# Performance work log

Hardware: AMD Instinct MI355X
Metric: run time of the kernel (lower is better)

Reference implementation:

```python
import jax, jax.numpy as jnp
import numpy as np

N = 40000          # nodes
E = 400000         # edges (avg degree 10)
MUL0, MUL1 = 64, 32   # 64x0e + 32x1o
RAD, HID = 8, 64      # fc_neurons = [8, 64]
WNUM = 192            # tp.weight_numel = 64+64+32+32
NUM_NEIGHBORS = 10.0
INV3 = 1.0 / np.sqrt(3.0)   # wigner coeff for 1o x 1o -> 0e


def _lin(s, v, Ws, Wv, attr):
    """FullyConnectedTensorProduct(x, 1x0e attr) == per-irrep linear, fan-in normalized."""
    out_s = (s @ Ws) * attr * (1.0 / np.sqrt(Ws.shape[0]))
    out_v = jnp.einsum('nud,uv->nvd', v, Wv) * attr[..., None] * (1.0 / np.sqrt(Wv.shape[0]))
    return out_s, out_v


def setup_inputs() -> dict:
    key = jax.random.key(0)
    ks = jax.random.split(key, 16)
    return {
        'node_input':   jax.random.normal(ks[0], (N, MUL0 + 3 * MUL1), jnp.float32),
        'node_attr':    jnp.ones((N, 1), jnp.float32),
        'edge_attr':    jax.random.normal(ks[1], (E, 4), jnp.float32),   # 1x0e + 1x1o
        'edge_scalars': jax.random.uniform(ks[2], (E, RAD), jnp.float32),
        'W_sc_s': jax.random.normal(ks[3], (MUL0, MUL0), jnp.float32),
        'W_sc_v': jax.random.normal(ks[4], (MUL1, MUL1), jnp.float32),
        'W1_s':   jax.random.normal(ks[5], (MUL0, MUL0), jnp.float32),
        'W1_v':   jax.random.normal(ks[6], (MUL1, MUL1), jnp.float32),
        'W2_s':   jax.random.normal(ks[7], (MUL0 + MUL1, MUL0), jnp.float32),
        'W2_v':   jax.random.normal(ks[8], (MUL0 + MUL1, MUL1), jnp.float32),
        'W3':     jax.random.normal(ks[9], (MUL0 + MUL1, 1), jnp.float32),
        'fcW1':   jax.random.normal(ks[10], (RAD, HID), jnp.float32),
        'fcW2':   jax.random.normal(ks[11], (HID, WNUM), jnp.float32),
        'edge_src': jax.random.randint(ks[12], (E,), 0, N, jnp.int32),
        'edge_dst': jax.random.randint(ks[13], (E,), 0, N, jnp.int32),
    }


def reference(node_input, node_attr, edge_attr, edge_scalars,
              W_sc_s, W_sc_v, W1_s, W1_v, W2_s, W2_v, W3, fcW1, fcW2,
              edge_src, edge_dst):
    n = node_input.shape[0]
    s_in = node_input[:, :MUL0]                       # (N, 64)   0e
    v_in = node_input[:, MUL0:].reshape(n, MUL1, 3)   # (N, 32,3) 1o

    # self connection + first linear (FCTP with 1x0e attr)
    sc_s, sc_v = _lin(s_in, v_in, W_sc_s, W_sc_v, node_attr)
    f_s,  f_v  = _lin(s_in, v_in, W1_s,  W1_v,  node_attr)

    # radial MLP -> per-edge tensor-product weights (silu, fan-in normalized)
    h = jax.nn.silu(edge_scalars @ fcW1 * (1.0 / np.sqrt(RAD)))
    w = h @ fcW2 * (1.0 / np.sqrt(HID))               # (E, 192)
    wA, wB, wC, wD = w[:, :64], w[:, 64:128], w[:, 128:160], w[:, 160:192]

    # gather source node features
    xs = f_s[edge_src]                                # (E, 64)
    xv = f_v[edge_src]                                # (E, 32, 3)
    y0 = edge_attr[:, :1]                             # (E, 1)  0e
    y1 = edge_attr[:, 1:4]                            # (E, 3)  1o

    # 'uvu' tensor-product paths -> irreps_mid = 64x0e + 32x0e + 64x1o + 32x1o
    outA = wA * xs * y0                                            # 0e x 0e -> 0e
    outD = wD * jnp.einsum('eud,ed->eu', xv, y1) * INV3            # 1o x 1o -> 0e
    outB = wB[:, :, None] * xs[:, :, None] * y1[:, None, :]       # 0e x 1o -> 1o
    outC = wC[:, :, None] * xv * y0[:, :, None]                    # 1o x 0e -> 1o
    edge_feat = jnp.concatenate(
        [outA, outD, outB.reshape(-1, MUL0 * 3), outC.reshape(-1, MUL1 * 3)], axis=1)  # (E, 384)

    # scatter_add into destination nodes, normalized by sqrt(num_neighbors)
    agg = jax.ops.segment_sum(edge_feat, edge_dst, num_segments=n)
    agg = agg * (1.0 / np.sqrt(NUM_NEIGHBORS))

    ms = agg[:, :MUL0 + MUL1]                               # (N, 96)   0e
    mv = agg[:, MUL0 + MUL1:].reshape(n, MUL0 + MUL1, 3)    # (N, 96,3) 1o

    # lin2: mid -> output ; lin3: mid -> 0e (scalars only)
    c_s, c_v = _lin(ms, mv, W2_s, W2_v, node_attr)
    conv = jnp.concatenate([c_s, c_v.reshape(n, -1)], axis=1)
    sc   = jnp.concatenate([sc_s, sc_v.reshape(n, -1)], axis=1)
    angle = 0.1 * (ms @ W3) * node_attr * (1.0 / np.sqrt(MUL0 + MUL1))  # (N, 1)

    # sc.output_mask is all-ones here (every output irrep has a path)
    cos, sin = jnp.cos(angle), jnp.sin(angle)
    return cos * sc + sin * conv
```

## Files before the change

kernel.cpp:

```cpp
#include <hip/hip_runtime.h>
#include <math.h>

#define MUL0 64
#define MUL1 32
#define RADF 8
#define HIDF 64
#define WNUM 192
#define NODE_F 160
#define AGG_F  384
#define SWS 200

#define INV_SQRT64 0.125f
#define INV_SQRT32 0.17677669529663687f
#define INV_SQRT8  0.35355339059327373f
#define INV_SQRT96 0.10206207261596575f
#define INV_SQRT10 0.31622776601683794f
#define INV_SQRT3  0.5773502691896258f

typedef __attribute__((ext_vector_type(8))) short bf16x8;
typedef __attribute__((ext_vector_type(4))) float f32x4;

__device__ __forceinline__ float bf2f(unsigned short u) {
    return __uint_as_float((unsigned)u << 16);
}
__device__ __forceinline__ unsigned short f2bfu(float x) {
    unsigned ua = __float_as_uint(x);
    return (unsigned short)((ua + 0x7FFF + ((ua >> 16) & 1)) >> 16);
}
__device__ __forceinline__ unsigned bf16pack(float a, float b) {
    unsigned ua = __float_as_uint(a);
    unsigned ub = __float_as_uint(b);
    ua = (ua + 0x7FFF + ((ua >> 16) & 1)) >> 16;
    ub = (ub + 0x7FFF + ((ub >> 16) & 1)) >> 16;
    return ua | (ub << 16);
}
__device__ __forceinline__ int rdlane(int v, int i) {
    return __builtin_amdgcn_readlane(v, i);
}
__device__ __forceinline__ bf16x8 cvt8(float4 a, float4 b) {
    union { unsigned q[4]; bf16x8 v; } r;
    r.q[0] = bf16pack(a.x, a.y);
    r.q[1] = bf16pack(a.z, a.w);
    r.q[2] = bf16pack(b.x, b.y);
    r.q[3] = bf16pack(b.z, b.w);
    return r.v;
}
__device__ __forceinline__ bf16x8 load8ovfb(const unsigned short* agn,
                                            const unsigned short* ovf16,
                                            int tA, int tB, int base)
{
    bf16x8 v = *(const bf16x8*)(agn + base);
    if (tA <= tB) {
        const unsigned short* pv = (const unsigned short*)&v;
        float f[8];
        #pragma unroll
        for (int j = 0; j < 8; ++j) f[j] = bf2f(pv[j]);
        for (int t = tA; t <= tB; ++t) {
            const unsigned short* ov = ovf16 + (size_t)t * AGG_F + base;
            #pragma unroll
            for (int j = 0; j < 8; ++j) f[j] += bf2f(ov[j]);
        }
        v = cvt8(make_float4(f[0], f[1], f[2], f[3]),
                 make_float4(f[4], f[5], f[6], f[7]));
    }
    return v;
}

__global__ __launch_bounds__(256) void k_node_lin(
    const float* __restrict__ node_input,
    const float* __restrict__ node_attr,
    const float* __restrict__ W1_s,
    const float* __restrict__ W1_v,
    unsigned short* __restrict__ f, int N)
{
    __shared__ unsigned short s_w1s[8 * 64 * 8];
    __shared__ unsigned short s_w1v[4 * 32 * 8];
    int tid = threadIdx.x;

    for (int task = tid; task < 8 * 64; task += 256) {
        int col = task & 63, koct = task >> 6;
        const float* wp = W1_s + (size_t)(koct * 8) * MUL0 + col;
        unsigned pk0 = bf16pack(wp[0 * MUL0] * INV_SQRT64, wp[1 * MUL0] * INV_SQRT64);
        unsigned pk1 = bf16pack(wp[2 * MUL0] * INV_SQRT64, wp[3 * MUL0] * INV_SQRT64);
        unsigned pk2 = bf16pack(wp[4 * MUL0] * INV_SQRT64, wp[5 * MUL0] * INV_SQRT64);
        unsigned pk3 = bf16pack(wp[6 * MUL0] * INV_SQRT64, wp[7 * MUL0] * INV_SQRT64);
        *(uint4*)&s_w1s[task * 8] = make_uint4(pk0, pk1, pk2, pk3);
    }
    for (int task = tid; task < 4 * 32; task += 256) {
        int col = task & 31, koct = task >> 5;
        const float* wp = W1_v + (size_t)(koct * 8) * MUL1 + col;
        unsigned pk0 = bf16pack(wp[0 * MUL1] * INV_SQRT32, wp[1 * MUL1] * INV_SQRT32);
        unsigned pk1 = bf16pack(wp[2 * MUL1] * INV_SQRT32, wp[3 * MUL1] * INV_SQRT32);
        unsigned pk2 = bf16pack(wp[4 * MUL1] * INV_SQRT32, wp[5 * MUL1] * INV_SQRT32);
        unsigned pk3 = bf16pack(wp[6 * MUL1] * INV_SQRT32, wp[7 * MUL1] * INV_SQRT32);
        *(uint4*)&s_w1v[task * 8] = make_uint4(pk0, pk1, pk2, pk3);
    }
    __syncthreads();

    int lane = tid & 63;
    int wv = tid >> 6;
    int l15 = lane & 15, lh = lane >> 4;
    int ntiles = (N + 15) >> 4;

    for (int tile = blockIdx.x * 4 + wv; tile < ntiles; tile += gridDim.x * 4) {
        int n0 = tile << 4;
        int m = min(16, N - n0);
        int nrow = n0 + min(l15, m - 1);
        const float* inn = node_input + (size_t)nrow * NODE_F;

        float attr[4];
        #pragma unroll
        for (int r = 0; r < 4; ++r)
            attr[r] = node_attr[n0 + min(lh * 4 + r, m - 1)];

        bf16x8 inS[2];
        #pragma unroll
        for (int kk = 0; kk < 2; ++kk) {
            const float* p0 = inn + kk * 32 + lh * 8;
            inS[kk] = cvt8(*(const float4*)p0, *(const float4*)(p0 + 4));
        }
        #pragma unroll
        for (int cb = 0; cb < 4; ++cb) {
            f32x4 a = {0.f, 0.f, 0.f, 0.f};
            #pragma unroll
            for (int kk = 0; kk < 2; ++kk) {
                bf16x8 b = *(const bf16x8*)&s_w1s[(((kk * 4 + lh) * 64) + cb * 16 + l15) * 8];
                a = __builtin_amdgcn_mfma_f32_16x16x32_bf16(inS[kk], b, a, 0, 0, 0);
            }
            #pragma unroll
            for (int r = 0; r < 4; ++r) {
                int node = lh * 4 + r;
                if (node < m)
                    f[(size_t)(n0 + node) * NODE_F + cb * 16 + l15] = f2bfu(a[r] * attr[r]);
            }
        }

        #pragma unroll
        for (int d = 0; d < 3; ++d) {
            float t[8];
            #pragma unroll
            for (int j = 0; j < 8; ++j)
                t[j] = inn[64 + (lh * 8 + j) * 3 + d];
            bf16x8 inV = cvt8(make_float4(t[0], t[1], t[2], t[3]),
                              make_float4(t[4], t[5], t[6], t[7]));
            #pragma unroll
            for (int cb = 0; cb < 2; ++cb) {
                bf16x8 b = *(const bf16x8*)&s_w1v[((lh * 32) + cb * 16 + l15) * 8];
                f32x4 a = {0.f, 0.f, 0.f, 0.f};
                a = __builtin_amdgcn_mfma_f32_16x16x32_bf16(inV, b, a, 0, 0, 0);
                #pragma unroll
                for (int r = 0; r < 4; ++r) {
                    int node = lh * 4 + r;
                    if (node < m)
                        f[(size_t)(n0 + node) * NODE_F + 64 + d * 32 + cb * 16 + l15] =
                            f2bfu(a[r] * attr[r]);
                }
            }
        }
    }
}

__global__ void k_count(const int* __restrict__ edge_dst, int* deg, int E)
{
    int e = blockIdx.x * blockDim.x + threadIdx.x;
    if (e < E) atomicAdd(&deg[edge_dst[e]], 1);
}

__global__ __launch_bounds__(1024) void k_scan_a(const int* __restrict__ deg,
                                                 int* __restrict__ off,
                                                 int* __restrict__ bsum, int N)
{
    __shared__ int swsum[16];
    __shared__ int swoff[16];
    __shared__ int stot;
    int lane = threadIdx.x & 63, wid = threadIdx.x >> 6;
    int ng4 = (N + 3) >> 2;
    int g = blockIdx.x * 1024 + threadIdx.x;
    int4 v = make_int4(0, 0, 0, 0);
    if (g < ng4) v = ((const int4*)deg)[g];
    int s = v.x + v.y + v.z + v.w;
    int val = s;
    #pragma unroll
    for (int sh = 1; sh < 64; sh <<= 1) {
        int t = __shfl_up(val, sh);
        if (lane >= sh) val += t;
    }
    if (lane == 63) swsum[wid] = val;
    __syncthreads();
    if (threadIdx.x < 16) {
        int x = swsum[threadIdx.x];
        int xv = x;
        #pragma unroll
        for (int sh = 1; sh < 16; sh <<= 1) {
            int t = __shfl_up(xv, sh);
            if ((int)threadIdx.x >= sh) xv += t;
        }
        swoff[threadIdx.x] = xv - x;
        if (threadIdx.x == 15) stot = xv;
    }
    __syncthreads();
    if (g < ng4) {
        int b0 = swoff[wid] + (val - s);
        int4 o;
        o.x = b0; o.y = b0 + v.x; o.z = o.y + v.y; o.w = o.z + v.z;
        ((int4*)off)[g] = o;
    }
    if (threadIdx.x == 0) bsum[blockIdx.x] = stot;
}

__global__ __launch_bounds__(1024) void k_scan_b(int* __restrict__ off,
                                                 int* __restrict__ cur,
                                                 const int* __restrict__ bsum,
                                                 unsigned short* __restrict__ agg,
                                                 const int* __restrict__ deg,
                                                 int N, int nb)
{
    __shared__ int sbase;
    if (threadIdx.x == 0) {
        int s = 0;
        for (int j = 0; j < (int)blockIdx.x; ++j) s += bsum[j];
        sbase = s;
    }
    __syncthreads();
    int base = sbase;
    int ng4 = (N + 3) >> 2;
    int g = blockIdx.x * 1024 + threadIdx.x;
    if (g < ng4) {
        int4 o = ((int4*)off)[g];
        o.x += base; o.y += base; o.z += base; o.w += base;
        ((int4*)off)[g] = o;
        ((int4*)cur)[g] = o;
        int4 d = ((const int4*)deg)[g];
        int n0 = g * 4;
        #pragma unroll
        for (int q = 0; q < 4; ++q) {
            int dq = (q == 0) ? d.x : (q == 1) ? d.y : (q == 2) ? d.z : d.w;
            int nq = n0 + q;
            if (dq == 0 && nq < N) {
                uint4* row = (uint4*)(agg + (size_t)nq * AGG_F);
                uint4 z = make_uint4(0, 0, 0, 0);
                for (int j = 0; j < AGG_F * 2 / 16; ++j) row[j] = z;
            }
        }
    }
}

__global__ void k_scatter(const int* __restrict__ edge_dst,
                          int* cur, int* __restrict__ csr, int E)
{
    int e = blockIdx.x * blockDim.x + threadIdx.x;
    if (e < E) {
        int d = edge_dst[e];
        int pos = atomicAdd(&cur[d], 1);
        csr[pos] = e;
    }
}

#define FLUSH_AGG(node, OVF)                                         \
    do {                                                             \
        unsigned short* an = (OVF) ? (ovf16 + (size_t)wt * AGG_F)    \
                                   : (agg + (size_t)(node) * AGG_F); \
        an[lane] = f2bfu(accA);                                      \
        an[96  + lane] = f2bfu(accB0);                               \
        an[192 + lane] = f2bfu(accB1);                               \
        an[288 + lane] = f2bfu(accB2);                               \
        if (lane < 32) {                                             \
            an[160 + u] = f2bfu(accX0);                              \
            an[256 + u] = f2bfu(accX1);                              \
            an[352 + u] = f2bfu(accX2);                              \
        } else {                                                     \
            an[64 + u] = f2bfu(accX0);                               \
        }                                                            \
    } while (0)

__global__ __launch_bounds__(512, 2) void k_edge_fused(
    const unsigned short* __restrict__ f,
    const float* __restrict__ edge_scalars,
    const float* __restrict__ edge_attr,
    const float* __restrict__ fcW1,
    const float* __restrict__ fcW2,
    const int* __restrict__ edge_src,
    const int* __restrict__ edge_dst,
    const int* __restrict__ csr,
    const int* __restrict__ off,
    unsigned short* __restrict__ agg,
    unsigned short* __restrict__ ovf16, int E)
{
    __shared__ unsigned short s_w2t[8 * 192 * 8];
    __shared__ unsigned short s_w[8][16 * SWS];
    __shared__ float s_fcW1[512];
    __shared__ float4 s_ea8[8][16];

    int tid  = threadIdx.x;
    int lane = tid & 63;
    int wv   = tid >> 6;
    int l15  = lane & 15, lh = lane >> 4;
    int u    = lane & 31;

    for (int task = tid; task < 1536; task += 512) {
        int col = task % 192, oct = task / 192;
        const float* wp = fcW2 + (size_t)(oct * 8) * WNUM + col;
        unsigned pk0 = bf16pack(wp[0 * WNUM], wp[1 * WNUM]);
        unsigned pk1 = bf16pack(wp[2 * WNUM], wp[3 * WNUM]);
        unsigned pk2 = bf16pack(wp[4 * WNUM], wp[5 * WNUM]);
        unsigned pk3 = bf16pack(wp[6 * WNUM], wp[7 * WNUM]);
        *(uint4*)&s_w2t[oct * 1536 + col * 8] = make_uint4(pk0, pk1, pk2, pk3);
    }
    for (int i = tid; i < 512; i += 512)
        s_fcW1[i] = fcW1[i];
    __syncthreads();

    unsigned short* sw = s_w[wv];
    float4* sea = s_ea8[wv];
    int nwt = (E + 15) >> 4;
    int stride8 = gridDim.x * 8;

    int wt = blockIdx.x * 8 + wv;
    if (wt >= nwt) return;

    int P = wt << 4;
    int m = min(16, E - P);
    int e0 = csr[P + min(l15, m - 1)];
    int src = edge_src[e0];
    int dst = edge_dst[e0];
    float4 ea = *(const float4*)(edge_attr + (size_t)e0 * 4);
    float4 es0, es1;
    {
        const float4* esp = (const float4*)(edge_scalars + (size_t)e0 * RADF);
        es0 = esp[0]; es1 = esp[1];
    }

    while (true) {
        if (lh == 0) sea[l15] = ea;

        int firstd = rdlane(dst, 0);
        int off_first = off[firstd];

        int wt_n = wt + stride8;
        bool hn = wt_n < nwt;
        int P_n = hn ? (wt_n << 4) : 0;
        int m_n = hn ? min(16, E - P_n) : 1;

        int e_n = csr[hn ? (P_n + min(l15, m_n - 1)) : 0];

        float xs[16], xv0[16], xv1[16], xv2[16];
        #pragma unroll
        for (int i = 0; i < 16; ++i) {
            int si = rdlane(src, i);
            const unsigned short* fb = f + (size_t)si * NODE_F;
            xs[i]  = bf2f(fb[lane]);
            xv0[i] = bf2f(fb[64 + u]);
            xv1[i] = bf2f(fb[96 + u]);
            xv2[i] = bf2f(fb[128 + u]);
        }

        float es[8] = {es0.x, es0.y, es0.z, es0.w, es1.x, es1.y, es1.z, es1.w};
        union { unsigned q[4]; bf16x8 v; } A0, A1;
        #pragma unroll
        for (int jp = 0; jp < 4; ++jp) {
            int k0 = lh * 8 + 2 * jp;
            float aL0 = 0.f, aL1 = 0.f, aH0 = 0.f, aH1 = 0.f;
            #pragma unroll
            for (int r = 0; r < 8; ++r) {
                float2 wl = *(const float2*)&s_fcW1[r * 64 + k0];
                float2 wh = *(const float2*)&s_fcW1[r * 64 + 32 + k0];
                aL0 = fmaf(es[r], wl.x, aL0);
                aL1 = fmaf(es[r], wl.y, aL1);
                aH0 = fmaf(es[r], wh.x, aH0);
                aH1 = fmaf(es[r], wh.y, aH1);
            }
            aL0 *= INV_SQRT8; aL1 *= INV_SQRT8; aH0 *= INV_SQRT8; aH1 *= INV_SQRT8;
            aL0 = aL0 / (1.f + __expf(-aL0));
            aL1 = aL1 / (1.f + __expf(-aL1));
            aH0 = aH0 / (1.f + __expf(-aH0));
            aH1 = aH1 / (1.f + __expf(-aH1));
            A0.q[jp] = bf16pack(aL0, aL1);
            A1.q[jp] = bf16pack(aH0, aH1);
        }

        int src_n = edge_src[e_n];
        int dst_n = edge_dst[e_n];
        float4 ea_n = *(const float4*)(edge_attr + (size_t)e_n * 4);
        float4 es0_n, es1_n;
        {
            const float4* espn = (const float4*)(edge_scalars + (size_t)e_n * RADF);
            es0_n = espn[0]; es1_n = espn[1];
        }

        #pragma unroll
        for (int cb = 0; cb < 12; ++cb) {
            bf16x8 b0 = *(const bf16x8*)&s_w2t[ lh      * 1536 + (cb * 16 + l15) * 8];
            bf16x8 b1 = *(const bf16x8*)&s_w2t[(4 + lh) * 1536 + (cb * 16 + l15) * 8];
            f32x4 acc = {0.f, 0.f, 0.f, 0.f};
            acc = __builtin_amdgcn_mfma_f32_16x16x32_bf16(A0.v, b0, acc, 0, 0, 0);
            acc = __builtin_amdgcn_mfma_f32_16x16x32_bf16(A1.v, b1, acc, 0, 0, 0);
            #pragma unroll
            for (int r = 0; r < 4; ++r)
                sw[(lh * 4 + r) * SWS + cb * 16 + l15] = f2bfu(acc[r] * INV_SQRT64);
        }

        float accA = 0.f, accB0 = 0.f, accB1 = 0.f, accB2 = 0.f;
        float accX0 = 0.f, accX1 = 0.f, accX2 = 0.f;
        int curd = rdlane(dst, 0);
        #pragma unroll
        for (int i = 0; i < 16; ++i) {
            if (i < m) {
                int di = rdlane(dst, i);
                if (di != curd) {
                    bool ov = (curd == firstd) && (off_first < P);
                    FLUSH_AGG(curd, ov);
                    accA = accB0 = accB1 = accB2 = 0.f;
                    accX0 = accX1 = accX2 = 0.f;
                    curd = di;
                }
                float4 eav = sea[i];
                float W0 = bf2f(sw[i * SWS + lane]);
                float W1 = bf2f(sw[i * SWS + 64 + lane]);
                float W2 = bf2f(sw[i * SWS + 128 + lane]);
                accA = fmaf(W0 * xs[i], eav.x, accA);
                float bx = W1 * xs[i];
                accB0 = fmaf(bx, eav.y, accB0);
                accB1 = fmaf(bx, eav.z, accB1);
                accB2 = fmaf(bx, eav.w, accB2);
                if (lane < 32) {
                    float cc = W2 * eav.x;
                    accX0 = fmaf(cc, xv0[i], accX0);
                    accX1 = fmaf(cc, xv1[i], accX1);
                    accX2 = fmaf(cc, xv2[i], accX2);
                } else {
                    float dv = xv0[i] * eav.y + xv1[i] * eav.z + xv2[i] * eav.w;
                    accX0 = fmaf(W2 * INV_SQRT3, dv, accX0);
                }
            }
        }
        {
            bool ov_fin = (curd == firstd) && (off_first < P);
            FLUSH_AGG(curd, ov_fin);
        }

        if (!hn) break;
        wt = wt_n; P = P_n; m = m_n;
        src = src_n; dst = dst_n; ea = ea_n; es0 = es0_n; es1 = es1_n;
    }
}

__global__ __launch_bounds__(256) void k_out(
    const float* __restrict__ node_input,
    const float* __restrict__ node_attr,
    const unsigned short* __restrict__ agg,
    const unsigned short* __restrict__ ovf16,
    const int* __restrict__ off,
    const float* __restrict__ W_sc_s,
    const float* __restrict__ W_sc_v,
    const float* __restrict__ W2_s,
    const float* __restrict__ W2_v,
    const float* __restrict__ W3,
    float* __restrict__ out, int N)
{
    __shared__ unsigned short s_w2s[12 * 64 * 8];
    __shared__ unsigned short s_wss[ 8 * 64 * 8];
    __shared__ unsigned short s_w2v[12 * 32 * 8];
    __shared__ unsigned short s_wsv[ 4 * 32 * 8];
    __shared__ unsigned short s_w3 [12 * 16 * 8];

    const float pre = INV_SQRT10 * INV_SQRT96;
    int tid = threadIdx.x;

    for (int task = tid; task < 12 * 64; task += 256) {
        int col = task & 63, koct = task >> 6;
        const float* wp = W2_s + (size_t)(koct * 8) * MUL0 + col;
        unsigned pk0 = bf16pack(wp[0 * MUL0] * pre, wp[1 * MUL0] * pre);
        unsigned pk1 = bf16pack(wp[2 * MUL0] * pre, wp[3 * MUL0] * pre);
        unsigned pk2 = bf16pack(wp[4 * MUL0] * pre, wp[5 * MUL0] * pre);
        unsigned pk3 = bf16pack(wp[6 * MUL0] * pre, wp[7 * MUL0] * pre);
        *(uint4*)&s_w2s[task * 8] = make_uint4(pk0, pk1, pk2, pk3);
    }
    for (int task = tid; task < 8 * 64; task += 256) {
        int col = task & 63, koct = task >> 6;
        const float* wp = W_sc_s + (size_t)(koct * 8) * MUL0 + col;
        unsigned pk0 = bf16pack(wp[0 * MUL0] * INV_SQRT64, wp[1 * MUL0] * INV_SQRT64);
        unsigned pk1 = bf16pack(wp[2 * MUL0] * INV_SQRT64, wp[3 * MUL0] * INV_SQRT64);
        unsigned pk2 = bf16pack(wp[4 * MUL0] * INV_SQRT64, wp[5 * MUL0] * INV_SQRT64);
        unsigned pk3 = bf16pack(wp[6 * MUL0] * INV_SQRT64, wp[7 * MUL0] * INV_SQRT64);
        *(uint4*)&s_wss[task * 8] = make_uint4(pk0, pk1, pk2, pk3);
    }
    for (int task = tid; task < 12 * 32; task += 256) {
        int col = task & 31, koct = task >> 5;
        const float* wp = W2_v + (size_t)(koct * 8) * MUL1 + col;
        unsigned pk0 = bf16pack(wp[0 * MUL1] * pre, wp[1 * MUL1] * pre);
        unsigned pk1 = bf16pack(wp[2 * MUL1] * pre, wp[3 * MUL1] * pre);
        unsigned pk2 = bf16pack(wp[4 * MUL1] * pre, wp[5 * MUL1] * pre);
        unsigned pk3 = bf16pack(wp[6 * MUL1] * pre, wp[7 * MUL1] * pre);
        *(uint4*)&s_w2v[task * 8] = make_uint4(pk0, pk1, pk2, pk3);
    }
    for (int task = tid; task < 4 * 32; task += 256) {
        int col = task & 31, koct = task >> 5;
        const float* wp = W_sc_v + (size_t)(koct * 8) * MUL1 + col;
        unsigned pk0 = bf16pack(wp[0 * MUL1] * INV_SQRT32, wp[1 * MUL1] * INV_SQRT32);
        unsigned pk1 = bf16pack(wp[2 * MUL1] * INV_SQRT32, wp[3 * MUL1] * INV_SQRT32);
        unsigned pk2 = bf16pack(wp[4 * MUL1] * INV_SQRT32, wp[5 * MUL1] * INV_SQRT32);
        unsigned pk3 = bf16pack(wp[6 * MUL1] * INV_SQRT32, wp[7 * MUL1] * INV_SQRT32);
        *(uint4*)&s_wsv[task * 8] = make_uint4(pk0, pk1, pk2, pk3);
    }
    for (int task = tid; task < 12 * 16; task += 256) {
        int col = task & 15, koct = task >> 4;
        const float sc3 = 0.1f * pre;
        unsigned pk0 = 0, pk1 = 0, pk2 = 0, pk3 = 0;
        if (col == 0) {
            const float* wp = W3 + koct * 8;
            pk0 = bf16pack(wp[0] * sc3, wp[1] * sc3);
            pk1 = bf16pack(wp[2] * sc3, wp[3] * sc3);
            pk2 = bf16pack(wp[4] * sc3, wp[5] * sc3);
            pk3 = bf16pack(wp[6] * sc3, wp[7] * sc3);
        }
        *(uint4*)&s_w3[task * 8] = make_uint4(pk0, pk1, pk2, pk3);
    }
    __syncthreads();

    int lane = tid & 63;
    int wv = tid >> 6;
    int l15 = lane & 15, lh = lane >> 4;
    int ntiles = (N + 15) >> 4;

    for (int tile = blockIdx.x * 4 + wv; tile < ntiles; tile += gridDim.x * 4) {
        int n0 = tile << 4;
        int m = min(16, N - n0);
        int nrow = n0 + min(l15, m - 1);
        const unsigned short* agn = agg + (size_t)nrow * AGG_F;
        const float* inn = node_input + (size_t)nrow * NODE_F;

        int o0 = off[nrow], o1 = off[nrow + 1];
        int tA = (o0 >> 4) + 1;
        int tB = (o1 > o0) ? ((o1 - 1) >> 4) : (tA - 1);

        bf16x8 aggA[3], inS[2];
        #pragma unroll
        for (int kk = 0; kk < 3; ++kk)
            aggA[kk] = load8ovfb(agn, ovf16, tA, tB, kk * 32 + lh * 8);
        #pragma unroll
        for (int kk = 0; kk < 2; ++kk) {
            const float* p0 = inn + kk * 32 + lh * 8;
            inS[kk] = cvt8(*(const float4*)p0, *(const float4*)(p0 + 4));
        }

        f32x4 convS[4], scS[4], angD = {0.f, 0.f, 0.f, 0.f};
        #pragma unroll
        for (int cb = 0; cb < 4; ++cb) {
            f32x4 a = {0.f, 0.f, 0.f, 0.f};
            #pragma unroll
            for (int kk = 0; kk < 3; ++kk) {
                bf16x8 b = *(const bf16x8*)&s_w2s[(((kk * 4 + lh) * 64) + cb * 16 + l15) * 8];
                a = __builtin_amdgcn_mfma_f32_16x16x32_bf16(aggA[kk], b, a, 0, 0, 0);
            }
            convS[cb] = a;
            f32x4 s = {0.f, 0.f, 0.f, 0.f};
            #pragma unroll
            for (int kk = 0; kk < 2; ++kk) {
                bf16x8 b = *(const bf16x8*)&s_wss[(((kk * 4 + lh) * 64) + cb * 16 + l15) * 8];
                s = __builtin_amdgcn_mfma_f32_16x16x32_bf16(inS[kk], b, s, 0, 0, 0);
            }
            scS[cb] = s;
        }
        #pragma unroll
        for (int kk = 0; kk < 3; ++kk) {
            bf16x8 b = *(const bf16x8*)&s_w3[(((kk * 4 + lh) * 16) + l15) * 8];
            angD = __builtin_amdgcn_mfma_f32_16x16x32_bf16(aggA[kk], b, angD, 0, 0, 0);
        }

        float attr[4], cs[4], sn[4];
        #pragma unroll
        for (int r = 0; r < 4; ++r) {
            attr[r] = node_attr[n0 + min(lh * 4 + r, m - 1)];
            float ang = __shfl(angD[r], lane & 48) * attr[r];
            cs[r] = cosf(ang);
            sn[r] = sinf(ang);
        }

        #pragma unroll
        for (int cb = 0; cb < 4; ++cb)
            #pragma unroll
            for (int r = 0; r < 4; ++r) {
                int node = lh * 4 + r;
                if (node < m)
                    out[(size_t)(n0 + node) * NODE_F + cb * 16 + l15] =
                        attr[r] * (cs[r] * scS[cb][r] + sn[r] * convS[cb][r]);
            }

        #pragma unroll
        for (int d = 0; d < 3; ++d) {
            bf16x8 aggV[3], inV;
            #pragma unroll
            for (int kk = 0; kk < 3; ++kk)
                aggV[kk] = load8ovfb(agn, ovf16, tA, tB, 96 + d * 96 + kk * 32 + lh * 8);
            {
                float t[8];
                #pragma unroll
                for (int j = 0; j < 8; ++j)
                    t[j] = inn[64 + (lh * 8 + j) * 3 + d];
                inV = cvt8(make_float4(t[0], t[1], t[2], t[3]),
                           make_float4(t[4], t[5], t[6], t[7]));
            }
            #pragma unroll
            for (int cb = 0; cb < 2; ++cb) {
                f32x4 a = {0.f, 0.f, 0.f, 0.f};
                #pragma unroll
                for (int kk = 0; kk < 3; ++kk) {
                    bf16x8 b = *(const bf16x8*)&s_w2v[(((kk * 4 + lh) * 32) + cb * 16 + l15) * 8];
                    a = __builtin_amdgcn_mfma_f32_16x16x32_bf16(aggV[kk], b, a, 0, 0, 0);
                }
                f32x4 s = {0.f, 0.f, 0.f, 0.f};
                {
                    bf16x8 b = *(const bf16x8*)&s_wsv[((lh * 32) + cb * 16 + l15) * 8];
                    s = __builtin_amdgcn_mfma_f32_16x16x32_bf16(inV, b, s, 0, 0, 0);
                }
                #pragma unroll
                for (int r = 0; r < 4; ++r) {
                    int node = lh * 4 + r;
                    if (node < m)
                        out[(size_t)(n0 + node) * NODE_F + 64 + (cb * 16 + l15) * 3 + d] =
                            attr[r] * (cs[r] * s[r] + sn[r] * a[r]);
                }
            }
        }
    }
}

extern "C" void kernel_launch(void* const* d_in, const int* in_sizes, int n_in,
                              void* d_out, int out_size, void* d_ws, size_t ws_size,
                              hipStream_t stream)
{
    const float* node_input   = (const float*)d_in[0];
    const float* node_attr    = (const float*)d_in[1];
    const float* edge_attr    = (const float*)d_in[2];
    const float* edge_scalars = (const float*)d_in[3];
    const float* W_sc_s       = (const float*)d_in[4];
    const float* W_sc_v       = (const float*)d_in[5];
    const float* W1_s         = (const float*)d_in[6];
    const float* W1_v         = (const float*)d_in[7];
    const float* W2_s         = (const float*)d_in[8];
    const float* W2_v         = (const float*)d_in[9];
    const float* W3           = (const float*)d_in[10];
    const float* fcW1         = (const float*)d_in[11];
    const float* fcW2         = (const float*)d_in[12];
    const int*   edge_src     = (const int*)d_in[13];
    const int*   edge_dst     = (const int*)d_in[14];
    float* out = (float*)d_out;

    const int N = in_sizes[1];
    const int E = in_sizes[13];
    const int Np = (N + 3) & ~3;
    const int nwt = (E + 15) / 16;

    char* p = (char*)d_ws;
    unsigned short* agg = (unsigned short*)p;  p += (size_t)N * AGG_F * sizeof(unsigned short);
    int*   deg = (int*)p;              p += (size_t)Np * sizeof(int);
    int*   cur = (int*)p;              p += (size_t)Np * sizeof(int);
    int*   off = (int*)p;              p += (size_t)(Np + 4) * sizeof(int);
    int*   csr = (int*)p;              p += (size_t)E * sizeof(int);
    int*   bsum = (int*)p;             p += 64 * sizeof(int);
    p = (char*)(((size_t)p + 15) & ~(size_t)15);
    unsigned short* ovf16 = (unsigned short*)p;

    unsigned short* fbf = (unsigned short*)d_out;

    hipMemsetAsync(deg, 0, (size_t)Np * sizeof(int), stream);

    int eb = (E + 255) / 256;
    k_count<<<eb, 256, 0, stream>>>(edge_dst, deg, E);

    int ng4 = (N + 3) >> 2;
    int nb = (ng4 + 1023) / 1024;
    k_scan_a<<<nb, 1024, 0, stream>>>(deg, off, bsum, N);
    k_scan_b<<<nb, 1024, 0, stream>>>(off, cur, bsum, agg, deg, N, nb);
    k_scatter<<<eb, 256, 0, stream>>>(edge_dst, cur, csr, E);

    int ntiles = (N + 15) / 16;
    int gridL = (ntiles + 3) / 4;
    k_node_lin<<<gridL, 256, 0, stream>>>(node_input, node_attr, W1_s, W1_v, fbf, N);

    int gridF = (nwt + 7) / 8;
    if (gridF > 1024) gridF = 1024;
    k_edge_fused<<<gridF, 512, 0, stream>>>(fbf, edge_scalars, edge_attr, fcW1, fcW2,
                                            edge_src, edge_dst, csr, off, agg, ovf16, E);

    int gridO = (ntiles + 3) / 4;
    if (gridO > 640) gridO = 640;
    k_out<<<gridO, 256, 0, stream>>>(node_input, node_attr, agg, ovf16, off,
                                     W_sc_s, W_sc_v, W2_s, W2_v, W3, out, N);
}
```

Before: 214.6 us.

## Split edge weight staging into three column phases to shrink LDS and raise occupancy

The fused edge kernel now computes the per-edge tensor-product weights in three 64-column chunks (A, B, C/D paths). Each chunk is staged into a smaller per-wave LDS buffer and consumed by its own segmented accumulation pass before the next chunk is computed. Destination indices are also staged in LDS so each pass can read them. The smaller LDS footprint and three live-accumulator groups are meant to allow three blocks per CU (launch bounds 512,3, grid capped at 768). In exchange it re-runs the segment-detection loop three times and issues more scattered partial-row stores.

```diff
diff --git a/kernel.cpp b/kernel.cpp
--- a/kernel.cpp
+++ b/kernel.cpp
@@ -8,7 +8,7 @@
 #define WNUM 192
 #define NODE_F 160
 #define AGG_F  384
-#define SWS 200
+#define SWQ 72
 
 #define INV_SQRT64 0.125f
 #define INV_SQRT32 0.17677669529663687f
@@ -256,24 +256,7 @@
     }
 }
 
-#define FLUSH_AGG(node, OVF)                                         \
-    do {                                                             \
-        unsigned short* an = (OVF) ? (ovf16 + (size_t)wt * AGG_F)    \
-                                   : (agg + (size_t)(node) * AGG_F); \
-        an[lane] = f2bfu(accA);                                      \
-        an[96  + lane] = f2bfu(accB0);                               \
-        an[192 + lane] = f2bfu(accB1);                               \
-        an[288 + lane] = f2bfu(accB2);                               \
-        if (lane < 32) {                                             \
-            an[160 + u] = f2bfu(accX0);                              \
-            an[256 + u] = f2bfu(accX1);                              \
-            an[352 + u] = f2bfu(accX2);                              \
-        } else {                                                     \
-            an[64 + u] = f2bfu(accX0);                               \
-        }                                                            \
-    } while (0)
-
-__global__ __launch_bounds__(512, 2) void k_edge_fused(
+__global__ __launch_bounds__(512, 3) void k_edge_fused(
     const unsigned short* __restrict__ f,
     const float* __restrict__ edge_scalars,
     const float* __restrict__ edge_attr,
@@ -287,9 +270,10 @@
     unsigned short* __restrict__ ovf16, int E)
 {
     __shared__ unsigned short s_w2t[8 * 192 * 8];
-    __shared__ unsigned short s_w[8][16 * SWS];
+    __shared__ unsigned short s_w[8][16 * SWQ];
     __shared__ float s_fcW1[512];
     __shared__ float4 s_ea8[8][16];
+    __shared__ int s_dst8[8][16];
 
     int tid  = threadIdx.x;
     int lane = tid & 63;
@@ -312,6 +296,7 @@
 
     unsigned short* sw = s_w[wv];
     float4* sea = s_ea8[wv];
+    int* sdst = s_dst8[wv];
     int nwt = (E + 15) >> 4;
     int stride8 = gridDim.x * 8;
 
@@ -331,10 +316,11 @@
     }
 
     while (true) {
-        if (lh == 0) sea[l15] = ea;
+        if (lh == 0) { sea[l15] = ea; sdst[l15] = dst; }
 
         int firstd = rdlane(dst, 0);
         int off_first = off[firstd];
+        bool ovf_head = off_first < P;
 
         int wt_n = wt + stride8;
         bool hn = wt_n < nwt;
@@ -388,7 +374,7 @@
         }
 
         #pragma unroll
-        for (int cb = 0; cb < 12; ++cb) {
+        for (int cb = 0; cb < 4; ++cb) {
             bf16x8 b0 = *(const bf16x8*)&s_w2t[ lh      * 1536 + (cb * 16 + l15) * 8];
             bf16x8 b1 = *(const bf16x8*)&s_w2t[(4 + lh) * 1536 + (cb * 16 + l15) * 8];
             f32x4 acc = {0.f, 0.f, 0.f, 0.f};
@@ -396,46 +382,127 @@
             acc = __builtin_amdgcn_mfma_f32_16x16x32_bf16(A1.v, b1, acc, 0, 0, 0);
             #pragma unroll
             for (int r = 0; r < 4; ++r)
-                sw[(lh * 4 + r) * SWS + cb * 16 + l15] = f2bfu(acc[r] * INV_SQRT64);
-        }
-
-        float accA = 0.f, accB0 = 0.f, accB1 = 0.f, accB2 = 0.f;
-        float accX0 = 0.f, accX1 = 0.f, accX2 = 0.f;
-        int curd = rdlane(dst, 0);
-        #pragma unroll
-        for (int i = 0; i < 16; ++i) {
-            if (i < m) {
-                int di = rdlane(dst, i);
-                if (di != curd) {
-                    bool ov = (curd == firstd) && (off_first < P);
-                    FLUSH_AGG(curd, ov);
-                    accA = accB0 = accB1 = accB2 = 0.f;
-                    accX0 = accX1 = accX2 = 0.f;
-                    curd = di;
+                sw[(lh * 4 + r) * SWQ + cb * 16 + l15] = f2bfu(acc[r] * INV_SQRT64);
+        }
+        {
+            float accA = 0.f;
+            int curd = firstd;
+            #pragma unroll
+            for (int i = 0; i < 16; ++i) {
+                if (i < m) {
+                    int di = sdst[i];
+                    if (di != curd) {
+                        bool ov = (curd == firstd) && ovf_head;
+                        unsigned short* an = ov ? (ovf16 + (size_t)wt * AGG_F)
+                                                : (agg + (size_t)curd * AGG_F);
+                        an[lane] = f2bfu(accA);
+                        accA = 0.f; curd = di;
+                    }
+                    accA = fmaf(bf2f(sw[i * SWQ + lane]) * xs[i], sea[i].x, accA);
                 }
-                float4 eav = sea[i];
-                float W0 = bf2f(sw[i * SWS + lane]);
-                float W1 = bf2f(sw[i * SWS + 64 + lane]);
-                float W2 = bf2f(sw[i * SWS + 128 + lane]);
-                accA = fmaf(W0 * xs[i], eav.x, accA);
-                float bx = W1 * xs[i];
-                accB0 = fmaf(bx, eav.y, accB0);
-                accB1 = fmaf(bx, eav.z, accB1);
-                accB2 = fmaf(bx, eav.w, accB2);
-                if (lane < 32) {
-                    float cc = W2 * eav.x;
-                    accX0 = fmaf(cc, xv0[i], accX0);
-                    accX1 = fmaf(cc, xv1[i], accX1);
-                    accX2 = fmaf(cc, xv2[i], accX2);
-                } else {
-                    float dv = xv0[i] * eav.y + xv1[i] * eav.z + xv2[i] * eav.w;
-                    accX0 = fmaf(W2 * INV_SQRT3, dv, accX0);
+            }
+            bool ov = (curd == firstd) && ovf_head;
+            unsigned short* an = ov ? (ovf16 + (size_t)wt * AGG_F)
+                                    : (agg + (size_t)curd * AGG_F);
+            an[lane] = f2bfu(accA);
+        }
+
+        #pragma unroll
+        for (int cb = 4; cb < 8; ++cb) {
+            bf16x8 b0 = *(const bf16x8*)&s_w2t[ lh      * 1536 + (cb * 16 + l15) * 8];
+            bf16x8 b1 = *(const bf16x8*)&s_w2t[(4 + lh) * 1536 + (cb * 16 + l15) * 8];
+            f32x4 acc = {0.f, 0.f, 0.f, 0.f};
+            acc = __builtin_amdgcn_mfma_f32_16x16x32_bf16(A0.v, b0, acc, 0, 0, 0);
+            acc = __builtin_amdgcn_mfma_f32_16x16x32_bf16(A1.v, b1, acc, 0, 0, 0);
+            #pragma unroll
+            for (int r = 0; r < 4; ++r)
+                sw[(lh * 4 + r) * SWQ + (cb - 4) * 16 + l15] = f2bfu(acc[r] * INV_SQRT64);
+        }
+        {
+            float accB0 = 0.f, accB1 = 0.f, accB2 = 0.f;
+            int curd = firstd;
+            #pragma unroll
+            for (int i = 0; i < 16; ++i) {
+                if (i < m) {
+                    int di = sdst[i];
+                    if (di != curd) {
+                        bool ov = (curd == firstd) && ovf_head;
+                        unsigned short* an = ov ? (ovf16 + (size_t)wt * AGG_F)
+                                                : (agg + (size_t)curd * AGG_F);
+                        an[96  + lane] = f2bfu(accB0);
+                        an[192 + lane] = f2bfu(accB1);
+                        an[288 + lane] = f2bfu(accB2);
+                        accB0 = accB1 = accB2 = 0.f; curd = di;
+                    }
+                    float4 eav = sea[i];
+                    float bx = bf2f(sw[i * SWQ + lane]) * xs[i];
+                    accB0 = fmaf(bx, eav.y, accB0);
+                    accB1 = fmaf(bx, eav.z, accB1);
+                    accB2 = fmaf(bx, eav.w, accB2);
                 }
             }
+            bool ov = (curd == firstd) && ovf_head;
+            unsigned short* an = ov ? (ovf16 + (size_t)wt * AGG_F)
+                                    : (agg + (size_t)curd * AGG_F);
+            an[96  + lane] = f2bfu(accB0);
+            an[192 + lane] = f2bfu(accB1);
+            an[288 + lane] = f2bfu(accB2);
+        }
+
+        #pragma unroll
+        for (int cb = 8; cb < 12; ++cb) {
+            bf16x8 b0 = *(const bf16x8*)&s_w2t[ lh      * 1536 + (cb * 16 + l15) * 8];
+            bf16x8 b1 = *(const bf16x8*)&s_w2t[(4 + lh) * 1536 + (cb * 16 + l15) * 8];
+            f32x4 acc = {0.f, 0.f, 0.f, 0.f};
+            acc = __builtin_amdgcn_mfma_f32_16x16x32_bf16(A0.v, b0, acc, 0, 0, 0);
+            acc = __builtin_amdgcn_mfma_f32_16x16x32_bf16(A1.v, b1, acc, 0, 0, 0);
+            #pragma unroll
+            for (int r = 0; r < 4; ++r)
+                sw[(lh * 4 + r) * SWQ + (cb - 8) * 16 + l15] = f2bfu(acc[r] * INV_SQRT64);
         }
         {
-            bool ov_fin = (curd == firstd) && (off_first < P);
-            FLUSH_AGG(curd, ov_fin);
+            float accX0 = 0.f, accX1 = 0.f, accX2 = 0.f;
+            int curd = firstd;
+            #pragma unroll
+            for (int i = 0; i < 16; ++i) {
+                if (i < m) {
+                    int di = sdst[i];
+                    if (di != curd) {
+                        bool ov = (curd == firstd) && ovf_head;
+                        unsigned short* an = ov ? (ovf16 + (size_t)wt * AGG_F)
+                                                : (agg + (size_t)curd * AGG_F);
+                        if (lane < 32) {
+                            an[160 + u] = f2bfu(accX0);
+                            an[256 + u] = f2bfu(accX1);
+                            an[352 + u] = f2bfu(accX2);
+                        } else {
+                            an[64 + u] = f2bfu(accX0);
+                        }
+                        accX0 = accX1 = accX2 = 0.f; curd = di;
+                    }
+                    float4 eav = sea[i];
+                    float W2 = bf2f(sw[i * SWQ + lane]);
+                    if (lane < 32) {
+                        float cc = W2 * eav.x;
+                        accX0 = fmaf(cc, xv0[i], accX0);
+                        accX1 = fmaf(cc, xv1[i], accX1);
+                        accX2 = fmaf(cc, xv2[i], accX2);
+                    } else {
+                        float dv = xv0[i] * eav.y + xv1[i] * eav.z + xv2[i] * eav.w;
+                        accX0 = fmaf(W2 * INV_SQRT3, dv, accX0);
+                    }
+                }
+            }
+            bool ov = (curd == firstd) && ovf_head;
+            unsigned short* an = ov ? (ovf16 + (size_t)wt * AGG_F)
+                                    : (agg + (size_t)curd * AGG_F);
+            if (lane < 32) {
+                an[160 + u] = f2bfu(accX0);
+                an[256 + u] = f2bfu(accX1);
+                an[352 + u] = f2bfu(accX2);
+            } else {
+                an[64 + u] = f2bfu(accX0);
+            }
         }
 
         if (!hn) break;
@@ -679,7 +746,7 @@
     k_node_lin<<<gridL, 256, 0, stream>>>(node_input, node_attr, W1_s, W1_v, fbf, N);
 
     int gridF = (nwt + 7) / 8;
-    if (gridF > 1024) gridF = 1024;
+    if (gridF > 768) gridF = 768;
     k_edge_fused<<<gridF, 512, 0, stream>>>(fbf, edge_scalars, edge_attr, fcW1, fcW2,
                                             edge_src, edge_dst, csr, off, agg, ovf16, E);
 
```

New measurement: 231.5 us. 7.9% more time.
